# Performance work log

Measured on AMD Instinct MI355X. Metric: run time of the kernel, lower is better.

Reference implementation:

```python
import jax, jax.numpy as jnp
import numpy as np

K = 9  # dynamic kernel size
PAD = K // 2


def conv2d(x, w, b):
    # x: (B,C,H,W), w: (O,I,3,3) 'SAME' padding, stride 1
    y = jax.lax.conv_general_dilated(
        x, w, window_strides=(1, 1), padding='SAME',
        dimension_numbers=('NCHW', 'OIHW', 'NCHW'))
    return y + b[None, :, None, None]


def setup_inputs() -> dict:
    key = jax.random.key(0)
    ks = jax.random.split(key, 8)
    B, H, W = 4, 384, 384
    rgb = jax.random.uniform(ks[0], (B, 3, H, W), dtype=jnp.float32)
    depth = jax.random.uniform(ks[1], (B, 1, H, W), dtype=jnp.float32)
    def he(k, shape):
        fan_in = shape[1] * shape[2] * shape[3]
        return jax.random.normal(k, shape, dtype=jnp.float32) * np.float32(np.sqrt(2.0 / fan_in))
    w1 = he(ks[2], (64, 4, 3, 3)); b1 = jnp.zeros((64,), jnp.float32)
    w2 = he(ks[3], (64, 64, 3, 3)); b2 = jnp.zeros((64,), jnp.float32)
    w3 = he(ks[4], (K * K, 64, 3, 3)); b3 = jnp.zeros((K * K,), jnp.float32)
    return {"rgb": rgb, "depth": depth, "w1": w1, "b1": b1,
            "w2": w2, "b2": b2, "w3": w3, "b3": b3}


def reference(rgb, depth, w1, b1, w2, b2, w3, b3):
    B, _, H, W = rgb.shape
    x = jnp.concatenate([rgb, depth], axis=1)  # (B,4,H,W)
    h = jax.nn.relu(conv2d(x, w1, b1))
    h = jax.nn.relu(conv2d(h, w2, b2))
    logits = conv2d(h, w3, b3)                 # (B,k*k,H,W)
    filters = jax.nn.softmax(logits, axis=1)   # softmax over k*k taps

    # im2col patches: (B, 3*k*k, H, W), channel-major (C outer, then kh, kw)
    patches = jax.lax.conv_general_dilated_patches(
        rgb, filter_shape=(K, K), window_strides=(1, 1),
        padding=[(PAD, PAD), (PAD, PAD)],
        dimension_numbers=('NCHW', 'OIHW', 'NCHW'))
    patches = patches.reshape(B, 3, K * K, H, W)

    bokeh = jnp.sum(patches * filters[:, None, :, :, :], axis=2)  # (B,3,H,W)
    return bokeh
```

## Files before the change

### kernel.cpp

```cpp
#include <hip/hip_runtime.h>
#include <hip/hip_fp16.h>

#define HH 384
#define WW 384
#define HWSZ (HH*WW)
#define NB 4

typedef _Float16 f16x8 __attribute__((ext_vector_type(8)));
typedef _Float16 f16x4 __attribute__((ext_vector_type(4)));
typedef _Float16 f16x2 __attribute__((ext_vector_type(2)));
typedef float    f32x4 __attribute__((ext_vector_type(4)));

#define W1A_B 75497472u
#define W2F_B (W1A_B + 9216u)
#define W3F_B (W2F_B + 73728u)

__global__ __launch_bounds__(256) void prep(const float* __restrict__ w1,
    const float* __restrict__ w2, const float* __restrict__ w3, char* __restrict__ ws) {
  int i = blockIdx.x * 256 + threadIdx.x;
  _Float16* w1a = (_Float16*)(ws + W1A_B);
  _Float16* w2f = (_Float16*)(ws + W2F_B);
  _Float16* w3f = (_Float16*)(ws + W3F_B);
  if (i < 4096) {
    int kstep = i >> 11, r = i & 2047;
    int ct = r >> 9, l = (r >> 3) & 63, j = i & 7;
    int k = kstep * 32 + (l >> 4) * 8 + j;
    int tap = k >> 2, ci = k & 3;
    int co = ct * 16 + (l & 15);
    w1a[i] = (tap < 9) ? (_Float16)w1[co * 36 + ci * 9 + tap] : (_Float16)0.f;
    return;
  }
  int o = i - 4096;
  if (o < 36864) {
    int cc = o / 18432, rem = o % 18432;
    int tap = rem >> 11, r2 = rem & 2047;
    int cj = r2 >> 9, l = (r2 >> 3) & 63, j = r2 & 7;
    int co = cj * 16 + (l & 15);
    int ci = cc * 32 + (l >> 4) * 8 + j;
    w2f[o] = (_Float16)w2[co * 576 + ci * 9 + tap];
    return;
  }
  o -= 36864;
  if (o < 55296) {
    int cc = o / 27648, rem = o % 27648;
    int tap = rem / 3072, r2 = rem % 3072;
    int cj = r2 >> 9, l = (r2 >> 3) & 63, j = r2 & 7;
    int co = cj * 16 + (l & 15);
    int ci = cc * 32 + (l >> 4) * 8 + j;
    w3f[o] = (co < 81) ? (_Float16)w3[co * 576 + ci * 9 + tap] : (_Float16)0.f;
  }
}

__global__ __launch_bounds__(256) void conv12(
    const float* __restrict__ rgb, const float* __restrict__ depth,
    const float* __restrict__ b1, const float* __restrict__ b2,
    const char* __restrict__ wsro, unsigned short* __restrict__ h2) {
  __shared__ __align__(16) char smem[36864];
  f16x2*    xwh = (f16x2*)smem;
  _Float16* h1T = (_Float16*)(smem + 3200);
  _Float16* w2l = (_Float16*)(smem + 23936);
  _Float16* tr  = (_Float16*)smem;
  const int t = threadIdx.x;
  const int x0 = blockIdx.x * 16, y0 = blockIdx.y * 16, b = blockIdx.z;
  const f16x8* w1af = (const f16x8*)(wsro + W1A_B);
  const _Float16* w2f = (const _Float16*)(wsro + W2F_B);
  const int lane = t & 63, q = lane >> 4, n = lane & 15, w = t >> 6;

  for (int idx = t; idx < 800; idx += 256) {
    int p = idx / 400, r2 = idx % 400, iy = r2 / 20, ix = r2 % 20;
    int gy = y0 + iy - 2, gx = x0 + ix - 2;
    f16x2 v = {(_Float16)0.f, (_Float16)0.f};
    if ((unsigned)gy < (unsigned)HH && (unsigned)gx < (unsigned)WW) {
      size_t off = (size_t)gy * WW + gx;
      int c0 = p * 2;
      float f0 = rgb[(size_t)(b * 3 + c0) * HWSZ + off];
      float f1 = (c0 + 1 < 3) ? rgb[(size_t)(b * 3 + c0 + 1) * HWSZ + off]
                              : depth[(size_t)b * HWSZ + off];
      v[0] = (_Float16)f0; v[1] = (_Float16)f1;
    }
    xwh[idx] = v;
  }

  f32x4 acc[4][4];
  #pragma unroll
  for (int cj = 0; cj < 4; ++cj) {
    float bv = b2[cj * 16 + n];
    #pragma unroll
    for (int ri = 0; ri < 4; ++ri) acc[ri][cj] = (f32x4){bv, bv, bv, bv};
  }
  __syncthreads();

  for (int cc = 0; cc < 2; ++cc) {
    {
      const float4* src = (const float4*)(w2f + cc * 18432);
      float4* dst = (float4*)w2l;
      for (int idx = t; idx < 768; idx += 256) dst[idx] = src[idx];
    }
    f16x8 wa[2][2];
    #pragma unroll
    for (int ks = 0; ks < 2; ++ks)
      #pragma unroll
      for (int c2 = 0; c2 < 2; ++c2)
        wa[ks][c2] = w1af[(ks * 4 + cc * 2 + c2) * 64 + lane];
    float4 bia[2];
    #pragma unroll
    for (int c2 = 0; c2 < 2; ++c2)
      bia[c2] = *(const float4*)&b1[(cc * 2 + c2) * 16 + q * 4];

    #pragma unroll 1
    for (int tile = w; tile < 21; tile += 4) {
      int px = tile * 16 + n;
      int pxc = px < 323 ? px : 323;
      int row = pxc / 18, col = pxc - row * 18;
      bool okp = ((unsigned)(y0 + row - 1) < (unsigned)HH) &&
                 ((unsigned)(x0 + col - 1) < (unsigned)WW);
      int t0 = q * 2, t1 = t0 + 1;
      int ky0 = t0 / 3, kx0 = t0 - ky0 * 3;
      int ky1 = t1 / 3, kx1 = t1 - ky1 * 3;
      f16x2 p00 = xwh[(row + ky0) * 20 + col + kx0];
      f16x2 p01 = xwh[400 + (row + ky0) * 20 + col + kx0];
      f16x2 p10 = xwh[(row + ky1) * 20 + col + kx1];
      f16x2 p11 = xwh[400 + (row + ky1) * 20 + col + kx1];
      f16x8 bf0 = {p00[0], p00[1], p01[0], p01[1], p10[0], p10[1], p11[0], p11[1]};
      f16x8 bf1 = {};
      if (q == 0) {
        f16x2 p80 = xwh[(row + 2) * 20 + col + 2];
        f16x2 p81 = xwh[400 + (row + 2) * 20 + col + 2];
        bf1[0] = p80[0]; bf1[1] = p80[1]; bf1[2] = p81[0]; bf1[3] = p81[1];
      }
      #pragma unroll
      for (int c2 = 0; c2 < 2; ++c2) {
        f32x4 a = (f32x4){bia[c2].x, bia[c2].y, bia[c2].z, bia[c2].w};
        a = __builtin_amdgcn_mfma_f32_16x16x32_f16(wa[0][c2], bf0, a, 0, 0, 0);
        a = __builtin_amdgcn_mfma_f32_16x16x32_f16(wa[1][c2], bf1, a, 0, 0, 0);
        if (px < 324) {
          f16x4 hv;
          #pragma unroll
          for (int i = 0; i < 4; ++i)
            hv[i] = okp ? (_Float16)fmaxf(a[i], 0.f) : (_Float16)0.f;
          int g = c2 * 2 + (q >> 1);
          *(f16x4*)&h1T[pxc * 32 + ((g ^ (col & 3)) * 8 + (q & 1) * 4)] = hv;
        }
      }
    }
    __syncthreads();

    #pragma unroll 1
    for (int tg = 0; tg < 3; ++tg) {
      #pragma unroll
      for (int tt = 0; tt < 3; ++tt) {
        f16x8 af[4];
        #pragma unroll
        for (int ri = 0; ri < 4; ++ri) {
          int row = w * 4 + ri + tg;
          int col = n + tt;
          af[ri] = *(const f16x8*)&h1T[(row * 18 + col) * 32 + ((q ^ (col & 3)) * 8)];
        }
        #pragma unroll
        for (int cj = 0; cj < 4; ++cj) {
          f16x8 bf = *(const f16x8*)&w2l[(tt * 4 + cj) * 512 + lane * 8];
          #pragma unroll
          for (int ri = 0; ri < 4; ++ri)
            acc[ri][cj] = __builtin_amdgcn_mfma_f32_16x16x32_f16(af[ri], bf, acc[ri][cj], 0, 0, 0);
        }
      }
      __syncthreads();
      if (tg < 2) {
        const float4* src = (const float4*)(w2f + cc * 18432 + (tg + 1) * 6144);
        float4* dst = (float4*)w2l;
        for (int idx = t; idx < 768; idx += 256) dst[idx] = src[idx];
        __syncthreads();
      }
    }
  }

  #pragma unroll
  for (int ri = 0; ri < 4; ++ri) {
    int py = w * 4 + ri;
    #pragma unroll
    for (int cj = 0; cj < 4; ++cj)
      #pragma unroll
      for (int i = 0; i < 4; ++i)
        tr[(py * 16 + q * 4 + i) * 72 + cj * 16 + n] = (_Float16)fmaxf(acc[ri][cj][i], 0.f);
  }
  __syncthreads();
  #pragma unroll
  for (int k = 0; k < 8; ++k) {
    int idx = t + k * 256;
    int y = idx >> 7, x = (idx >> 3) & 15, c8 = (idx & 7) * 8;
    f16x8 v = *(const f16x8*)&tr[(y * 16 + x) * 72 + c8];
    *(f16x8*)&h2[(((size_t)b * HH + y0 + y) * WW + x0 + x) * 64 + c8] = v;
  }
}

__global__ __launch_bounds__(512) void conv3bokeh(
    const unsigned short* __restrict__ h2, const float* __restrict__ rgb,
    const float* __restrict__ b3, const char* __restrict__ wsro,
    float* __restrict__ out) {
  __shared__ __align__(16) char smem[40224];
  _Float16* h2T  = (_Float16*)smem;
  _Float16* w3l  = (_Float16*)(smem + 20736);
  float*    rgbl = (float*)(smem + 33024);
  const int t = threadIdx.x;
  const int x0 = blockIdx.x * 16, y0 = blockIdx.y * 16, b = blockIdx.z;
  const _Float16* w3f = (const _Float16*)(wsro + W3F_B);
  const int lane = t & 63, q = lane >> 4, n = lane & 15, w = t >> 6;

  f32x4 acc[2][6];
  #pragma unroll
  for (int mt = 0; mt < 6; ++mt)
    #pragma unroll
    for (int i = 0; i < 4; ++i) {
      float bv = 0.f;
      if (mt < 5) bv = b3[mt * 16 + q * 4 + i];
      else if (q == 0 && i == 0) bv = b3[80];
      acc[0][mt][i] = bv;
      acc[1][mt][i] = bv;
    }

  float4 wr;
  if (t < 384) wr = ((const float4*)w3f)[t];

  for (int idx = t; idx < 1728; idx += 512) {
    int c = idx / 576, r2 = idx % 576, ry = r2 / 24, rx = r2 % 24;
    int gy = y0 + ry - 4, gx = x0 + rx - 4;
    float v = 0.f;
    if ((unsigned)gy < (unsigned)HH && (unsigned)gx < (unsigned)WW)
      v = rgb[(size_t)(b * 3 + c) * HWSZ + gy * WW + gx];
    rgbl[c * 600 + ry * 25 + rx] = v;
  }

  auto stageH2 = [&](int cc) {
    for (int idx = t; idx < 1296; idx += 512) {
      int g = idx & 3, pc = idx >> 2;
      int row = pc / 18, col = pc - row * 18;
      int gy = y0 + row - 1, gx = x0 + col - 1;
      f16x8 v = {};
      if ((unsigned)gy < (unsigned)HH && (unsigned)gx < (unsigned)WW)
        v = *(const f16x8*)&h2[(((size_t)b * HH + gy) * WW + gx) * 64 + cc * 32 + g * 8];
      *(f16x8*)&h2T[(row * 18 + col) * 32 + ((g ^ (col & 3)) * 8)] = v;
    }
  };
  stageH2(0);

  if (t < 384) *(float4*)(w3l + t * 8) = wr;
  __syncthreads();

  #pragma unroll 1
  for (int cc = 0; cc < 2; ++cc) {
    #pragma unroll 1
    for (int tap = 0; tap < 9; ++tap) {
      const int k = cc * 9 + tap;
      const int cur = k & 1;
      if (k < 17 && t < 384) wr = ((const float4*)(w3f + (k + 1) * 3072))[t];

      const _Float16* wcur = w3l + cur * 3072;
      const int ty = tap / 3, tx = tap - ty * 3;
      f16x8 bf0, bf1;
      {
        int row0 = w * 2 + ty, col = n + tx;
        int sw = (q ^ (col & 3)) * 8;
        bf0 = *(const f16x8*)&h2T[(row0 * 18 + col) * 32 + sw];
        bf1 = *(const f16x8*)&h2T[((row0 + 1) * 18 + col) * 32 + sw];
      }
      __builtin_amdgcn_s_setprio(1);
      #pragma unroll
      for (int mt = 0; mt < 6; ++mt) {
        f16x8 af = *(const f16x8*)&wcur[(mt * 64 + lane) * 8];
        acc[0][mt] = __builtin_amdgcn_mfma_f32_16x16x32_f16(af, bf0, acc[0][mt], 0, 0, 0);
        acc[1][mt] = __builtin_amdgcn_mfma_f32_16x16x32_f16(af, bf1, acc[1][mt], 0, 0, 0);
      }
      __builtin_amdgcn_s_setprio(0);
      if (k < 17 && t < 384) *(float4*)(w3l + (1 - cur) * 3072 + t * 8) = wr;
      if (k == 8) {
        __syncthreads();
        stageH2(1);
      }
      __syncthreads();
    }
  }

  #pragma unroll
  for (int ri = 0; ri < 2; ++ri) {
    const int ry0 = w * 2 + ri;
    float m = -1e30f;
    #pragma unroll
    for (int mt = 0; mt < 5; ++mt)
      #pragma unroll
      for (int i = 0; i < 4; ++i) m = fmaxf(m, acc[ri][mt][i]);
    if (q == 0) m = fmaxf(m, acc[ri][5][0]);
    m = fmaxf(m, __shfl_xor(m, 16));
    m = fmaxf(m, __shfl_xor(m, 32));
    float s = 0.f, a0 = 0.f, a1 = 0.f, a2 = 0.f;
    #pragma unroll
    for (int mt = 0; mt < 5; ++mt) {
      int t0 = mt * 16 + q * 4;
      int ty = t0 / 9, tx = t0 - ty * 9;
      int base = (ry0 + ty) * 25 + n + tx;
      #pragma unroll
      for (int i = 0; i < 4; ++i) {
        int adr = base + i + ((tx + i > 8) ? 16 : 0);
        float e = __expf(acc[ri][mt][i] - m);
        s += e;
        a0 = fmaf(e, rgbl[adr], a0);
        a1 = fmaf(e, rgbl[600 + adr], a1);
        a2 = fmaf(e, rgbl[1200 + adr], a2);
      }
    }
    if (q == 0) {
      float e = __expf(acc[ri][5][0] - m);
      s += e;
      int adr = (ry0 + 8) * 25 + n + 8;
      a0 = fmaf(e, rgbl[adr], a0);
      a1 = fmaf(e, rgbl[600 + adr], a1);
      a2 = fmaf(e, rgbl[1200 + adr], a2);
    }
    #pragma unroll
    for (int st = 16; st < 64; st <<= 1) {
      s  += __shfl_xor(s, st);
      a0 += __shfl_xor(a0, st);
      a1 += __shfl_xor(a1, st);
      a2 += __shfl_xor(a2, st);
    }
    if (q == 0) {
      float inv = 1.f / s;
      size_t o = (size_t)b * 3 * HWSZ + (size_t)(y0 + ry0) * WW + (x0 + n);
      out[o] = a0 * inv;
      out[o + HWSZ] = a1 * inv;
      out[o + 2 * HWSZ] = a2 * inv;
    }
  }
}

extern "C" void kernel_launch(void* const* d_in, const int* in_sizes, int n_in,
                              void* d_out, int out_size, void* d_ws, size_t ws_size,
                              hipStream_t stream) {
  const float* rgb   = (const float*)d_in[0];
  const float* depth = (const float*)d_in[1];
  const float* w1    = (const float*)d_in[2];
  const float* b1    = (const float*)d_in[3];
  const float* w2    = (const float*)d_in[4];
  const float* b2    = (const float*)d_in[5];
  const float* w3    = (const float*)d_in[6];
  const float* b3    = (const float*)d_in[7];
  char* ws = (char*)d_ws;
  unsigned short* h2 = (unsigned short*)d_ws;
  float* out = (float*)d_out;

  prep<<<376, 256, 0, stream>>>(w1, w2, w3, ws);

  dim3 grid(WW / 16, HH / 16, NB);
  conv12<<<grid, 256, 0, stream>>>(rgb, depth, b1, b2, ws, h2);
  conv3bokeh<<<grid, 512, 0, stream>>>(h2, rgb, b3, ws, out);
}
```

Before: 213.3 us.

## Permute conv3 output channels, stream weights via global_load_lds, interleave rgb tile

```diff
diff --git a/kernel.cpp b/kernel.cpp
--- a/kernel.cpp
+++ b/kernel.cpp
@@ -14,6 +14,15 @@
 #define W1A_B 75497472u
 #define W2F_B (W1A_B + 9216u)
 #define W3F_B (W2F_B + 73728u)
+
+__device__ __forceinline__ int perm_oc(int g, int i, bool& valid) {
+  valid = true;
+  if (g < 18) return (g >> 1) * 9 + (g & 1) * 4 + i;
+  if (g == 18) return i * 9 + 8;
+  if (g == 19) return 44 + 9 * i;
+  if (g == 20) { valid = (i == 0); return 80; }
+  valid = false; return 0;
+}
 
 __global__ __launch_bounds__(256) void prep(const float* __restrict__ w1,
     const float* __restrict__ w2, const float* __restrict__ w3, char* __restrict__ ws) {
@@ -45,9 +54,11 @@
     int cc = o / 27648, rem = o % 27648;
     int tap = rem / 3072, r2 = rem % 3072;
     int cj = r2 >> 9, l = (r2 >> 3) & 63, j = r2 & 7;
-    int co = cj * 16 + (l & 15);
+    int p = cj * 16 + (l & 15);
     int ci = cc * 32 + (l >> 4) * 8 + j;
-    w3f[o] = (co < 81) ? (_Float16)w3[co * 576 + ci * 9 + tap] : (_Float16)0.f;
+    bool valid;
+    int oc = perm_oc(p >> 2, p & 3, valid);
+    w3f[o] = valid ? (_Float16)w3[oc * 576 + ci * 9 + tap] : (_Float16)0.f;
   }
 }
 
@@ -206,20 +217,29 @@
   const _Float16* w3f = (const _Float16*)(wsro + W3F_B);
   const int lane = t & 63, q = lane >> 4, n = lane & 15, w = t >> 6;
 
+  const int wof = __builtin_amdgcn_readfirstlane(w * 1024);
+  if (w < 6) {
+    const char* gsrc = (const char*)w3f + (size_t)t * 16;
+    __builtin_amdgcn_global_load_lds(
+        (const __attribute__((address_space(1))) void*)gsrc,
+        (__attribute__((address_space(3))) void*)((char*)w3l + wof), 16, 0, 0);
+  }
+
   f32x4 acc[2][6];
   #pragma unroll
   for (int mt = 0; mt < 6; ++mt)
     #pragma unroll
     for (int i = 0; i < 4; ++i) {
       float bv = 0.f;
-      if (mt < 5) bv = b3[mt * 16 + q * 4 + i];
-      else if (q == 0 && i == 0) bv = b3[80];
+      if (mt < 5) {
+        int g = mt * 4 + q;
+        int oc = (g < 18) ? (g >> 1) * 9 + (g & 1) * 4 + i
+                          : ((g == 18) ? i * 9 + 8 : 44 + 9 * i);
+        bv = b3[oc];
+      } else if (q == 0 && i == 0) bv = b3[80];
       acc[0][mt][i] = bv;
       acc[1][mt][i] = bv;
     }
-
-  float4 wr;
-  if (t < 384) wr = ((const float4*)w3f)[t];
 
   for (int idx = t; idx < 1728; idx += 512) {
     int c = idx / 576, r2 = idx % 576, ry = r2 / 24, rx = r2 % 24;
@@ -227,7 +247,7 @@
     float v = 0.f;
     if ((unsigned)gy < (unsigned)HH && (unsigned)gx < (unsigned)WW)
       v = rgb[(size_t)(b * 3 + c) * HWSZ + gy * WW + gx];
-    rgbl[c * 600 + ry * 25 + rx] = v;
+    rgbl[ry * 75 + c * 25 + rx] = v;
   }
 
   auto stageH2 = [&](int cc) {
@@ -242,8 +262,6 @@
     }
   };
   stageH2(0);
-
-  if (t < 384) *(float4*)(w3l + t * 8) = wr;
   __syncthreads();
 
   #pragma unroll 1
@@ -252,7 +270,13 @@
     for (int tap = 0; tap < 9; ++tap) {
       const int k = cc * 9 + tap;
       const int cur = k & 1;
-      if (k < 17 && t < 384) wr = ((const float4*)(w3f + (k + 1) * 3072))[t];
+      if (k < 17 && w < 6) {
+        const char* gsrc = (const char*)(w3f + (k + 1) * 3072) + (size_t)t * 16;
+        __builtin_amdgcn_global_load_lds(
+            (const __attribute__((address_space(1))) void*)gsrc,
+            (__attribute__((address_space(3))) void*)((char*)w3l + (1 - cur) * 6144 + wof),
+            16, 0, 0);
+      }
 
       const _Float16* wcur = w3l + cur * 3072;
       const int ty = tap / 3, tx = tap - ty * 3;
@@ -271,7 +295,6 @@
         acc[1][mt] = __builtin_amdgcn_mfma_f32_16x16x32_f16(af, bf1, acc[1][mt], 0, 0, 0);
       }
       __builtin_amdgcn_s_setprio(0);
-      if (k < 17 && t < 384) *(float4*)(w3l + (1 - cur) * 3072 + t * 8) = wr;
       if (k == 8) {
         __syncthreads();
         stageH2(1);
@@ -294,26 +317,42 @@
     float s = 0.f, a0 = 0.f, a1 = 0.f, a2 = 0.f;
     #pragma unroll
     for (int mt = 0; mt < 5; ++mt) {
-      int t0 = mt * 16 + q * 4;
-      int ty = t0 / 9, tx = t0 - ty * 9;
-      int base = (ry0 + ty) * 25 + n + tx;
+      float e[4];
       #pragma unroll
       for (int i = 0; i < 4; ++i) {
-        int adr = base + i + ((tx + i > 8) ? 16 : 0);
-        float e = __expf(acc[ri][mt][i] - m);
-        s += e;
-        a0 = fmaf(e, rgbl[adr], a0);
-        a1 = fmaf(e, rgbl[600 + adr], a1);
-        a2 = fmaf(e, rgbl[1200 + adr], a2);
+        e[i] = __expf(acc[ri][mt][i] - m);
+        s += e[i];
+      }
+      if (mt < 4) {
+        int dy = mt * 2 + (q >> 1);
+        int base = (ry0 + dy) * 75 + n + (q & 1) * 4;
+        #pragma unroll
+        for (int i = 0; i < 4; ++i) {
+          a0 = fmaf(e[i], rgbl[base + i], a0);
+          a1 = fmaf(e[i], rgbl[base + 25 + i], a1);
+          a2 = fmaf(e[i], rgbl[base + 50 + i], a2);
+        }
+      } else {
+        int dy = (q < 2) ? 8 : (q - 2) * 4;
+        int dx = (q < 2) ? q * 4 : 8;
+        int st = (q < 2) ? 1 : 75;
+        int base = (ry0 + dy) * 75 + n + dx;
+        #pragma unroll
+        for (int i = 0; i < 4; ++i) {
+          int adr = base + i * st;
+          a0 = fmaf(e[i], rgbl[adr], a0);
+          a1 = fmaf(e[i], rgbl[adr + 25], a1);
+          a2 = fmaf(e[i], rgbl[adr + 50], a2);
+        }
       }
     }
     if (q == 0) {
       float e = __expf(acc[ri][5][0] - m);
       s += e;
-      int adr = (ry0 + 8) * 25 + n + 8;
-      a0 = fmaf(e, rgbl[adr], a0);
-      a1 = fmaf(e, rgbl[600 + adr], a1);
-      a2 = fmaf(e, rgbl[1200 + adr], a2);
+      int base = (ry0 + 8) * 75 + n + 8;
+      a0 = fmaf(e, rgbl[base], a0);
+      a1 = fmaf(e, rgbl[base + 25], a1);
+      a2 = fmaf(e, rgbl[base + 50], a2);
     }
     #pragma unroll
     for (int st = 16; st < 64; st <<= 1) {
```

New measurement: 207.8 us, median of 2. 1.03x faster.
